# Performance work log

Measured on AMD Instinct MI355X. Metric: run time of the kernel, lower is better.

Reference implementation:

```python
import jax, jax.numpy as jnp
import numpy as np

N, E = 50000, 800000
H_IN, H, L = 256, 128, 3
EPS = 1e-5  # BatchNorm1d default eps


def setup_inputs() -> dict:
    key = jax.random.key(0)
    ks = jax.random.split(key, 8)
    x = jax.random.normal(ks[0], (N, H_IN), jnp.float32)
    edge_index = jax.random.randint(ks[1], (2, E), 0, N, dtype=jnp.int32)

    def glorot(k, fi, fo):
        lim = np.sqrt(6.0 / (fi + fo)).astype(np.float32)
        return jax.random.uniform(k, (fi, fo), jnp.float32, -lim, lim)

    W_feat = glorot(ks[2], H_IN, H)
    b_feat = jnp.zeros((H,), jnp.float32)
    wkeys = jax.random.split(ks[3], L)
    Ws = jnp.stack([glorot(wkeys[i], H, H) for i in range(L)])
    bs = jnp.zeros((L, H), jnp.float32)
    # BN init per reset_parameters: weight=1, bias=1e-4
    bn_feat_g = jnp.ones((H_IN,), jnp.float32)
    bn_feat_b = jnp.full((H_IN,), 1e-4, jnp.float32)
    bn_g = jnp.ones((L, H), jnp.float32)
    bn_b = jnp.full((L, H), 1e-4, jnp.float32)
    return dict(x=x, edge_index=edge_index, bn_feat_g=bn_feat_g, bn_feat_b=bn_feat_b,
                W_feat=W_feat, b_feat=b_feat, bn_g=bn_g, bn_b=bn_b, Ws=Ws, bs=bs)


def _bn(x, gamma, beta):
    # training-mode BatchNorm1d: batch statistics over nodes, biased variance
    mu = x.mean(0)
    var = x.var(0)
    return (x - mu) * jax.lax.rsqrt(var + EPS) * gamma + beta


def _gcn_norm(edge_index, n):
    # add self-loops (fill value 1) + symmetric deg^-1/2 normalization
    row, col = edge_index[0], edge_index[1]
    loop = jnp.arange(n, dtype=row.dtype)
    row = jnp.concatenate([row, loop])
    col = jnp.concatenate([col, loop])
    deg = jax.ops.segment_sum(jnp.ones_like(row, jnp.float32), row, num_segments=n)
    dinv = jnp.where(deg > 0, jax.lax.rsqrt(deg), 0.0)
    return row, col, dinv[row] * dinv[col]


def _gcn(x, W, b, row, col, norm, n):
    x = x @ W                                   # [n, out]
    msg = x[row] * norm[:, None]                # gather + scale, [E+n, out]
    out = jax.ops.segment_sum(msg, col, num_segments=n)  # scatter-add
    return out + b


def reference(x, edge_index, bn_feat_g, bn_feat_b, W_feat, b_feat, bn_g, bn_b, Ws, bs):
    n = x.shape[0]
    row, col, norm = _gcn_norm(edge_index, n)   # same for every layer
    x = _bn(x, bn_feat_g, bn_feat_b)
    x = _gcn(x, W_feat, b_feat, row, col, norm, n)
    for i in range(L):
        x = _bn(x, bn_g[i], bn_b[i])
        x = _gcn(x, Ws[i], bs[i], row, col, norm, n)
    return x
```

## Files before the change

kernel.cpp:

```cpp
#include <hip/hip_runtime.h>
#include <hip/hip_bf16.h>

#define H_IN 256
#define H    128
#define BN_EPS 1e-5f
#define NCOPY 32
#define NSLICE 256
#define SMAX 5120
#define STATS_FLOATS (NCOPY * 2 * H_IN)
#define SBLK 512
#define GEMMB 512

using u16 = unsigned short;
using u32 = unsigned int;
typedef __attribute__((ext_vector_type(8))) unsigned short us8;
typedef __attribute__((ext_vector_type(8))) short bf16x8;
typedef __attribute__((ext_vector_type(4))) float f32x4;

__device__ __forceinline__ float b2f(u16 u) {
    return __uint_as_float(((u32)u) << 16);
}
__device__ __forceinline__ u16 f2b(float f) {
    u32 u = __float_as_uint(f);
    u += 0x7FFF + ((u >> 16) & 1);
    return (u16)(u >> 16);
}

__global__ __launch_bounds__(256) void build_k(const int* __restrict__ row,
                                               const int* __restrict__ col,
                                               u32* __restrict__ deg,
                                               u32* __restrict__ bcnt_part,
                                               const float* __restrict__ x,
                                               u16* __restrict__ xb,
                                               float* __restrict__ statsA,
                                               int E, int total4) {
    int tid = threadIdx.x;
    if (blockIdx.x < NSLICE) {
        __shared__ u32 bcnt[256];
        bcnt[tid] = 0;
        __syncthreads();
        int len = (E + NSLICE - 1) / NSLICE;
        int e0 = blockIdx.x * len;
        int e1 = min(e0 + len, E);
        for (int e = e0 + tid; e < e1; e += 256) {
            atomicAdd(&deg[(u32)row[e]], 1u);
            atomicAdd(&bcnt[((u32)col[e]) >> 8], 1u);
        }
        __syncthreads();
        bcnt_part[blockIdx.x * 256 + tid] = bcnt[tid];
    } else {
        __shared__ float sh[2 * H_IN];
        const int K = H_IN;
        const int csz = 2 * H_IN;
        sh[tid] = 0.f;
        sh[tid + 256] = 0.f;
        __syncthreads();
        int gid = (blockIdx.x - NSLICE) * 256 + tid;
        int stride = SBLK * 256;
        int c0 = (gid * 4) % K;
        float s0=0.f,s1=0.f,s2=0.f,s3=0.f, q0=0.f,q1=0.f,q2=0.f,q3=0.f;
        const float4* A4 = (const float4*)x;
        ushort4* X4 = (ushort4*)xb;
        for (int i = gid; i < total4; i += stride) {
            float4 v = A4[i];
            ushort4 xv;
            xv.x = f2b(v.x); xv.y = f2b(v.y); xv.z = f2b(v.z); xv.w = f2b(v.w);
            X4[i] = xv;
            s0 += v.x; q0 += v.x * v.x;
            s1 += v.y; q1 += v.y * v.y;
            s2 += v.z; q2 += v.z * v.z;
            s3 += v.w; q3 += v.w * v.w;
        }
        atomicAdd(&sh[c0],     s0); atomicAdd(&sh[K + c0],     q0);
        atomicAdd(&sh[c0 + 1], s1); atomicAdd(&sh[K + c0 + 1], q1);
        atomicAdd(&sh[c0 + 2], s2); atomicAdd(&sh[K + c0 + 2], q2);
        atomicAdd(&sh[c0 + 3], s3); atomicAdd(&sh[K + c0 + 3], q3);
        __syncthreads();
        float* dst = statsA + (size_t)((blockIdx.x - NSLICE) & (NCOPY - 1)) * csz;
        for (int i = tid; i < csz; i += 256) atomicAdd(&dst[i], sh[i]);
    }
}

__global__ __launch_bounds__(256) void prep_k(const int* __restrict__ row,
                                              const int* __restrict__ col,
                                              const u32* __restrict__ bcnt_part,
                                              u32* __restrict__ bbase,
                                              u32* __restrict__ ebuf,
                                              const u32* __restrict__ deg,
                                              float* __restrict__ dinv,
                                              const float* __restrict__ W,
                                              const float* __restrict__ stats_mc,
                                              const float* __restrict__ g,
                                              const float* __restrict__ bcoef,
                                              const float* __restrict__ bias,
                                              u16* __restrict__ Wt,
                                              float* __restrict__ bp,
                                              int E, int N, int DB) {
    int tid = threadIdx.x;
    int bx = blockIdx.x;
    if (bx < NSLICE) {
        __shared__ u32 sc[256];
        __shared__ u32 cur[256];
        int s = bx;
        u32 tot = 0, pre = 0;
        for (int t = 0; t < NSLICE; ++t) {
            u32 v = bcnt_part[t * 256 + tid];
            tot += v;
            if (t < s) pre += v;
        }
        sc[tid] = tot;
        __syncthreads();
        for (int o = 1; o < 256; o <<= 1) {
            u32 xv = (tid >= o) ? sc[tid - o] : 0;
            __syncthreads();
            sc[tid] += xv;
            __syncthreads();
        }
        u32 base = sc[tid] - tot;
        if (s == 0) {
            bbase[tid] = base;
            if (tid == 255) bbase[256] = sc[255];
        }
        cur[tid] = base + pre;
        __syncthreads();
        int len = (E + NSLICE - 1) / NSLICE;
        int e0 = s * len;
        int e1 = min(e0 + len, E);
        for (int e = e0 + tid; e < e1; e += 256) {
            u32 r = (u32)row[e];
            u32 c = (u32)col[e];
            u32 pos = atomicAdd(&cur[c >> 8], 1u);
            ebuf[pos] = r | ((c & 255u) << 16);
        }
    } else if (bx < NSLICE + DB) {
        int n = (bx - NSLICE) * 256 + tid;
        if (n < N) dinv[n] = rsqrtf((float)deg[n] + 1.0f);
    } else {
        int j = bx - NSLICE - DB;
        int k = tid;
        const int K = H_IN;
        const int csz = 2 * H_IN;
        float sum = 0.f, sumsq = 0.f;
#pragma unroll
        for (int c = 0; c < NCOPY; ++c) {
            sum   += stats_mc[(size_t)c * csz + k];
            sumsq += stats_mc[(size_t)c * csz + K + k];
        }
        float mu = sum / (float)N;
        float var = sumsq / (float)N - mu * mu;
        float sK = g[k] * rsqrtf(var + BN_EPS);
        float tK = bcoef[k] - mu * sK;
        float w = W[(size_t)k * H + j];
        Wt[(size_t)j * K + k] = f2b(sK * w);
        __shared__ float red[256];
        red[k] = tK * w;
        __syncthreads();
        for (int o = 128; o > 0; o >>= 1) {
            if (k < o) red[k] += red[k + o];
            __syncthreads();
        }
        if (k == 0) bp[j] = bias[j] + red[0];
    }
}

__global__ void fold_k(const float* __restrict__ W, const float* __restrict__ stats_mc,
                       const float* __restrict__ g, const float* __restrict__ b,
                       const float* __restrict__ bias, u16* __restrict__ Wt,
                       float* __restrict__ bp, int N, int K) {
    int j = blockIdx.x;
    int k = threadIdx.x;
    int csz = 2 * K;
    float sum = 0.f, sumsq = 0.f;
#pragma unroll
    for (int c = 0; c < NCOPY; ++c) {
        sum   += stats_mc[(size_t)c * csz + k];
        sumsq += stats_mc[(size_t)c * csz + K + k];
    }
    float mu = sum / (float)N;
    float var = sumsq / (float)N - mu * mu;
    float s = g[k] * rsqrtf(var + BN_EPS);
    float t = b[k] - mu * s;
    float w = W[(size_t)k * H + j];
    Wt[(size_t)j * K + k] = f2b(s * w);
    __shared__ float red[256];
    red[k] = t * w;
    __syncthreads();
    for (int o = blockDim.x >> 1; o > 0; o >>= 1) {
        if (k < o) red[k] += red[k + o];
        __syncthreads();
    }
    if (k == 0) bp[j] = bias[j] + red[0];
}

template<int KT, int WITH_SORT>
__global__ __launch_bounds__(256) void gemm_mfma_k(const u16* __restrict__ Ab,
                                                   const u16* __restrict__ Wt,
                                                   u16* __restrict__ Yb, int M,
                                                   float* __restrict__ stats_z,
                                                   const u32* __restrict__ ebuf,
                                                   const u32* __restrict__ bbase,
                                                   int* __restrict__ rowptr,
                                                   u16* __restrict__ esrc, int N) {
    int tid = threadIdx.x;
    if constexpr (WITH_SORT != 0) {
        if (blockIdx.x >= GEMMB) {
            __shared__ u32 est[SMAX];
            __shared__ u32 hist[256], scanv[256], cur[256];
            int b = blockIdx.x - GEMMB;
            u32 base = bbase[b];
            int size = (int)(bbase[b + 1] - base);
            int st = min(size, SMAX);
            hist[tid] = 0;
            __syncthreads();
            for (int i = tid; i < st; i += 256) {
                u32 e = ebuf[base + i];
                est[i] = e;
                atomicAdd(&hist[(e >> 16) & 255u], 1u);
            }
            for (int i = SMAX + tid; i < size; i += 256) {
                u32 e = ebuf[base + i];
                atomicAdd(&hist[(e >> 16) & 255u], 1u);
            }
            __syncthreads();
            u32 own = hist[tid];
            scanv[tid] = own;
            __syncthreads();
            for (int o = 1; o < 256; o <<= 1) {
                u32 t = (tid >= o) ? scanv[tid - o] : 0;
                __syncthreads();
                scanv[tid] += t;
                __syncthreads();
            }
            u32 excl = scanv[tid] - own;
            int idx = (b << 8) + tid;
            if (idx <= N) rowptr[idx] = (int)(base + excl);
            cur[tid] = excl;
            __syncthreads();
            for (int i = tid; i < st; i += 256) {
                u32 e = est[i];
                u32 pos = atomicAdd(&cur[(e >> 16) & 255u], 1u);
                esrc[base + pos] = (u16)(e & 0xFFFFu);
            }
            for (int i = SMAX + tid; i < size; i += 256) {
                u32 e = ebuf[base + i];
                u32 pos = atomicAdd(&cur[(e >> 16) & 255u], 1u);
                esrc[base + pos] = (u16)(e & 0xFFFFu);
            }
            return;
        }
    }
    const int K = KT * 32;
    if (stats_z && blockIdx.x == 0) {
        for (int i = tid; i < STATS_FLOATS; i += 256) stats_z[i] = 0.f;
    }
    int w = tid >> 6;
    int lane = tid & 63;
    int m16 = lane & 15;
    int q = lane >> 4;

    bf16x8 bfrag[KT][2];
#pragma unroll
    for (int t = 0; t < KT; ++t)
#pragma unroll
        for (int p = 0; p < 2; ++p) {
            int ncol = 32 * w + 16 * p + m16;
            bfrag[t][p] = *(const bf16x8*)(Wt + (size_t)ncol * K + 32 * t + 8 * q);
        }

    int nchunk = M >> 4;
    for (int c = blockIdx.x; c < nchunk; c += GEMMB) {
        int m0 = c << 4;
        const u16* Arow = Ab + (size_t)(m0 + m16) * K + 8 * q;
        bf16x8 afrag[KT];
#pragma unroll
        for (int t = 0; t < KT; ++t)
            afrag[t] = *(const bf16x8*)(Arow + 32 * t);
        f32x4 acc0 = {0.f, 0.f, 0.f, 0.f}, acc1 = {0.f, 0.f, 0.f, 0.f};
#pragma unroll
        for (int t = 0; t < KT; ++t) {
            acc0 = __builtin_amdgcn_mfma_f32_16x16x32_bf16(afrag[t], bfrag[t][0], acc0, 0, 0, 0);
            acc1 = __builtin_amdgcn_mfma_f32_16x16x32_bf16(afrag[t], bfrag[t][1], acc1, 0, 0, 0);
        }
        u16* Crow = Yb + (size_t)(m0 + q * 4) * H + 32 * w + m16;
#pragma unroll
        for (int i = 0; i < 4; ++i) {
            Crow[(size_t)i * H]      = f2b(acc0[i]);
            Crow[(size_t)i * H + 16] = f2b(acc1[i]);
        }
    }
}

__global__ __launch_bounds__(256) void csragg_k(const int* __restrict__ rowptr,
                                                const u16* __restrict__ esrc,
                                                const u16* __restrict__ Yb,
                                                const float* __restrict__ dinv,
                                                const float* __restrict__ bp,
                                                u16* __restrict__ Ob,
                                                float* __restrict__ Of,
                                                float* __restrict__ stats_mc,
                                                int do_stats, int N) {
    __shared__ float sh[1024];
    int tid = threadIdx.x;
    int node = blockIdx.x * 16 + (tid >> 4);
    int fl = tid & 15;
    float o[8] = {0.f,0.f,0.f,0.f,0.f,0.f,0.f,0.f};
    if (node < N) {
        const us8* Y8 = (const us8*)Yb;
        float dn = dinv[node];
        float acc[8];
        {
            us8 ys = Y8[(size_t)node * 16 + fl];
#pragma unroll
            for (int j = 0; j < 8; ++j) acc[j] = dn * b2f(ys[j]);
        }
        int s = rowptr[node], e = rowptr[node + 1];
        int p = s;
        for (; p + 3 < e; p += 4) {
            int s0 = esrc[p], s1 = esrc[p + 1], s2 = esrc[p + 2], s3 = esrc[p + 3];
            float n0 = dinv[s0], n1 = dinv[s1], n2 = dinv[s2], n3 = dinv[s3];
            us8 v0 = Y8[(size_t)s0 * 16 + fl];
            us8 v1 = Y8[(size_t)s1 * 16 + fl];
            us8 v2 = Y8[(size_t)s2 * 16 + fl];
            us8 v3 = Y8[(size_t)s3 * 16 + fl];
#pragma unroll
            for (int j = 0; j < 8; ++j) acc[j] += n0 * b2f(v0[j]);
#pragma unroll
            for (int j = 0; j < 8; ++j) acc[j] += n1 * b2f(v1[j]);
#pragma unroll
            for (int j = 0; j < 8; ++j) acc[j] += n2 * b2f(v2[j]);
#pragma unroll
            for (int j = 0; j < 8; ++j) acc[j] += n3 * b2f(v3[j]);
        }
        for (; p < e; ++p) {
            int s0 = esrc[p];
            float n0 = dinv[s0];
            us8 v0 = Y8[(size_t)s0 * 16 + fl];
#pragma unroll
            for (int j = 0; j < 8; ++j) acc[j] += n0 * b2f(v0[j]);
        }
        float4 b0 = ((const float4*)bp)[fl * 2];
        float4 b1 = ((const float4*)bp)[fl * 2 + 1];
        o[0] = b0.x + dn * acc[0]; o[1] = b0.y + dn * acc[1];
        o[2] = b0.z + dn * acc[2]; o[3] = b0.w + dn * acc[3];
        o[4] = b1.x + dn * acc[4]; o[5] = b1.y + dn * acc[5];
        o[6] = b1.z + dn * acc[6]; o[7] = b1.w + dn * acc[7];
        if (Of) {
            float4* O4 = (float4*)Of;
            O4[(size_t)node * 32 + fl * 2]     = make_float4(o[0], o[1], o[2], o[3]);
            O4[(size_t)node * 32 + fl * 2 + 1] = make_float4(o[4], o[5], o[6], o[7]);
        } else {
            us8 ov;
#pragma unroll
            for (int j = 0; j < 8; ++j) ov[j] = f2b(o[j]);
            *(us8*)(Ob + (size_t)node * H + fl * 8) = ov;
        }
    }
    if (do_stats) {
        float sv[16];
#pragma unroll
        for (int j = 0; j < 8; ++j) { sv[j] = o[j]; sv[8 + j] = o[j] * o[j]; }
#pragma unroll
        for (int j = 0; j < 16; ++j) {
            sv[j] += __shfl_xor(sv[j], 16, 64);
            sv[j] += __shfl_xor(sv[j], 32, 64);
        }
        int lane = tid & 63, wv = tid >> 6;
        if (lane < 16) {
            float* base = sh + wv * 256;
#pragma unroll
            for (int j = 0; j < 8; ++j) {
                base[fl * 8 + j]       = sv[j];
                base[128 + fl * 8 + j] = sv[8 + j];
            }
        }
        __syncthreads();
        float v = sh[tid] + sh[256 + tid] + sh[512 + tid] + sh[768 + tid];
        atomicAdd(&stats_mc[(size_t)(blockIdx.x & (NCOPY - 1)) * (2 * H) + tid], v);
    }
}

extern "C" void kernel_launch(void* const* d_in, const int* in_sizes, int n_in,
                              void* d_out, int out_size, void* d_ws, size_t ws_size,
                              hipStream_t stream) {
    const float* x     = (const float*)d_in[0];
    const int*   ei    = (const int*)d_in[1];
    const float* bnfg  = (const float*)d_in[2];
    const float* bnfb  = (const float*)d_in[3];
    const float* Wfeat = (const float*)d_in[4];
    const float* bfeat = (const float*)d_in[5];
    const float* bng   = (const float*)d_in[6];
    const float* bnb   = (const float*)d_in[7];
    const float* Ws    = (const float*)d_in[8];
    const float* bs    = (const float*)d_in[9];

    int N = in_sizes[0] / H_IN;
    int E = in_sizes[1] / 2;
    const int* row = ei;
    const int* col = ei + E;

    int NB = (N + 255) >> 8;

    char* p = (char*)d_ws;
    auto alloc = [&](size_t bytes) { char* r = p; p += (bytes + 63) & ~size_t(63); return r; };
    float* statsA    = (float*)alloc(STATS_FLOATS * 4);
    float* statsB    = (float*)alloc(STATS_FLOATS * 4);
    u32*   deg       = (u32*)alloc((size_t)N * 4);
    float* dinv      = (float*)alloc((size_t)N * 4);
    u16*   Wt        = (u16*)alloc(H_IN * H * 2);
    float* bp        = (float*)alloc(H * 4);
    u32*   bcnt_part = (u32*)alloc(NSLICE * 256 * 4);
    u32*   bbase     = (u32*)alloc(257 * 4);
    int*   rowptr    = (int*)alloc((size_t)(N + 1) * 4);
    u32*   ebuf      = (u32*)alloc((size_t)E * 4);
    u16*   esrc      = (u16*)alloc((size_t)E * 2);
    u16*   xb        = (u16*)alloc((size_t)N * H_IN * 2);
    u16*   Yb        = (u16*)alloc((size_t)N * H * 2);
    u16*   ACTb      = (u16*)alloc((size_t)N * H * 2);

    float* out = (float*)d_out;

    hipMemsetAsync(statsA, 0, (size_t)(2 * STATS_FLOATS) * 4 + (size_t)N * 4, stream);

    build_k<<<NSLICE + SBLK, 256, 0, stream>>>(row, col, deg, bcnt_part, x, xb, statsA,
                                               E, N * H_IN / 4);
    prep_k<<<NSLICE + NB + H, 256, 0, stream>>>(row, col, bcnt_part, bbase, ebuf, deg, dinv,
                                                Wfeat, statsA, bnfg, bnfb, bfeat, Wt, bp,
                                                E, N, NB);
    gemm_mfma_k<8, 1><<<GEMMB + NB, 256, 0, stream>>>(xb, Wt, Yb, N, nullptr,
                                                      ebuf, bbase, rowptr, esrc, N);
    csragg_k<<<(N + 15) / 16, 256, 0, stream>>>(rowptr, esrc, Yb, dinv, bp,
                                                ACTb, nullptr, statsB, 1, N);

    for (int l = 1; l < 4; ++l) {
        const float* W    = Ws + (size_t)(l - 1) * H * H;
        const float* bias = bs + (size_t)(l - 1) * H;
        const float* g    = bng + (size_t)(l - 1) * H;
        const float* bb   = bnb + (size_t)(l - 1) * H;
        float* sfold   = (l & 1) ? statsB : statsA;
        float* szero   = (l == 1) ? statsA : (l == 2) ? statsB : nullptr;
        float* starget = ((l + 1) & 1) ? statsB : statsA;

        fold_k<<<H, H, 0, stream>>>(W, sfold, g, bb, bias, Wt, bp, N, H);
        gemm_mfma_k<4, 0><<<GEMMB, 256, 0, stream>>>(ACTb, Wt, Yb, N, szero,
                                                     nullptr, nullptr, nullptr, nullptr, N);
        csragg_k<<<(N + 15) / 16, 256, 0, stream>>>(rowptr, esrc, Yb, dinv, bp,
                                                    ACTb, (l == 3) ? out : nullptr,
                                                    starget, (l < 3) ? 1 : 0, N);
    }
}
```

Baseline: 394.9 us.

## Replace global degree atomics with sliced shared-memory 16-bit packed histograms

New measurement: 358.1 us. 1.1x faster.

```diff
diff --git a/kernel.cpp b/kernel.cpp
--- a/kernel.cpp
+++ b/kernel.cpp
@@ -6,6 +6,8 @@
 #define BN_EPS 1e-5f
 #define NCOPY 32
 #define NSLICE 256
+#define HSL 32
+#define QWMAX 8192
 #define SMAX 5120
 #define STATS_FLOATS (NCOPY * 2 * H_IN)
 #define SBLK 512
@@ -28,36 +30,56 @@
 
 __global__ __launch_bounds__(256) void build_k(const int* __restrict__ row,
                                                const int* __restrict__ col,
-                                               u32* __restrict__ deg,
+                                               u32* __restrict__ hist_part,
                                                u32* __restrict__ bcnt_part,
                                                const float* __restrict__ x,
                                                u16* __restrict__ xb,
                                                float* __restrict__ statsA,
-                                               int E, int total4) {
+                                               int E, int total4, int QW, int qN) {
+    __shared__ u32 smem[QWMAX];
     int tid = threadIdx.x;
-    if (blockIdx.x < NSLICE) {
-        __shared__ u32 bcnt[256];
+    int bx = blockIdx.x;
+    if (bx < NSLICE) {
+        u32* bcnt = smem;
         bcnt[tid] = 0;
         __syncthreads();
         int len = (E + NSLICE - 1) / NSLICE;
-        int e0 = blockIdx.x * len;
+        int e0 = bx * len;
         int e1 = min(e0 + len, E);
+        for (int e = e0 + tid; e < e1; e += 256)
+            atomicAdd(&bcnt[((u32)col[e]) >> 8], 1u);
+        __syncthreads();
+        bcnt_part[bx * 256 + tid] = bcnt[tid];
+    } else if (bx < NSLICE + 4 * HSL) {
+        int hb = bx - NSLICE;
+        int s = hb >> 2;
+        int qq = hb & 3;
+        u32* hist = smem;
+        for (int i = tid; i < QW; i += 256) hist[i] = 0;
+        __syncthreads();
+        int len = (E + HSL - 1) / HSL;
+        int e0 = s * len;
+        int e1 = min(e0 + len, E);
+        int lo = qq * qN;
         for (int e = e0 + tid; e < e1; e += 256) {
-            atomicAdd(&deg[(u32)row[e]], 1u);
-            atomicAdd(&bcnt[((u32)col[e]) >> 8], 1u);
-        }
-        __syncthreads();
-        bcnt_part[blockIdx.x * 256 + tid] = bcnt[tid];
+            int r = row[e] - lo;
+            if ((u32)r < (u32)qN)
+                atomicAdd(&hist[r >> 1], 1u << ((r & 1) << 4));
+        }
+        __syncthreads();
+        u32* dst = hist_part + (size_t)hb * QW;
+        for (int i = tid; i < QW; i += 256) dst[i] = hist[i];
     } else {
-        __shared__ float sh[2 * H_IN];
+        float* sh = (float*)smem;
         const int K = H_IN;
         const int csz = 2 * H_IN;
         sh[tid] = 0.f;
         sh[tid + 256] = 0.f;
         __syncthreads();
-        int gid = (blockIdx.x - NSLICE) * 256 + tid;
+        int sb = bx - NSLICE - 4 * HSL;
+        int gid = sb * 256 + tid;
         int stride = SBLK * 256;
-        int c0 = (gid * 4) % K;
+        int c0 = (gid * 4) & (H_IN - 1);
         float s0=0.f,s1=0.f,s2=0.f,s3=0.f, q0=0.f,q1=0.f,q2=0.f,q3=0.f;
         const float4* A4 = (const float4*)x;
         ushort4* X4 = (ushort4*)xb;
@@ -76,7 +98,7 @@
         atomicAdd(&sh[c0 + 2], s2); atomicAdd(&sh[K + c0 + 2], q2);
         atomicAdd(&sh[c0 + 3], s3); atomicAdd(&sh[K + c0 + 3], q3);
         __syncthreads();
-        float* dst = statsA + (size_t)((blockIdx.x - NSLICE) & (NCOPY - 1)) * csz;
+        float* dst = statsA + (size_t)(sb & (NCOPY - 1)) * csz;
         for (int i = tid; i < csz; i += 256) atomicAdd(&dst[i], sh[i]);
     }
 }
@@ -86,7 +108,7 @@
                                               const u32* __restrict__ bcnt_part,
                                               u32* __restrict__ bbase,
                                               u32* __restrict__ ebuf,
-                                              const u32* __restrict__ deg,
+                                              const u32* __restrict__ hist_part,
                                               float* __restrict__ dinv,
                                               const float* __restrict__ W,
                                               const float* __restrict__ stats_mc,
@@ -95,7 +117,7 @@
                                               const float* __restrict__ bias,
                                               u16* __restrict__ Wt,
                                               float* __restrict__ bp,
-                                              int E, int N, int DB) {
+                                              int E, int N, int DB, int QW, int qN) {
     int tid = threadIdx.x;
     int bx = blockIdx.x;
     if (bx < NSLICE) {
@@ -133,8 +155,17 @@
             ebuf[pos] = r | ((c & 255u) << 16);
         }
     } else if (bx < NSLICE + DB) {
-        int n = (bx - NSLICE) * 256 + tid;
-        if (n < N) dinv[n] = rsqrtf((float)deg[n] + 1.0f);
+        int w = (bx - NSLICE) * 256 + tid;
+        if (w < 4 * QW) {
+            int qq = w / QW;
+            int lw = w - qq * QW;
+            u32 v = 0;
+            for (int s = 0; s < HSL; ++s)
+                v += hist_part[(size_t)(s * 4 + qq) * QW + lw];
+            int n = qq * qN + 2 * lw;
+            if (n < N)     dinv[n]     = rsqrtf((float)(v & 0xFFFF) + 1.0f);
+            if (n + 1 < N) dinv[n + 1] = rsqrtf((float)(v >> 16) + 1.0f);
+        }
     } else {
         int j = bx - NSLICE - DB;
         int k = tid;
@@ -399,15 +430,18 @@
     const int* col = ei + E;
 
     int NB = (N + 255) >> 8;
+    int QW = (N + 7) / 8;
+    int qN = 2 * QW;
+    int DB = (4 * QW + 255) / 256;
 
     char* p = (char*)d_ws;
     auto alloc = [&](size_t bytes) { char* r = p; p += (bytes + 63) & ~size_t(63); return r; };
     float* statsA    = (float*)alloc(STATS_FLOATS * 4);
     float* statsB    = (float*)alloc(STATS_FLOATS * 4);
-    u32*   deg       = (u32*)alloc((size_t)N * 4);
     float* dinv      = (float*)alloc((size_t)N * 4);
     u16*   Wt        = (u16*)alloc(H_IN * H * 2);
     float* bp        = (float*)alloc(H * 4);
+    u32*   hist_part = (u32*)alloc((size_t)4 * HSL * QW * 4);
     u32*   bcnt_part = (u32*)alloc(NSLICE * 256 * 4);
     u32*   bbase     = (u32*)alloc(257 * 4);
     int*   rowptr    = (int*)alloc((size_t)(N + 1) * 4);
@@ -419,13 +453,15 @@
 
     float* out = (float*)d_out;
 
-    hipMemsetAsync(statsA, 0, (size_t)(2 * STATS_FLOATS) * 4 + (size_t)N * 4, stream);
-
-    build_k<<<NSLICE + SBLK, 256, 0, stream>>>(row, col, deg, bcnt_part, x, xb, statsA,
-                                               E, N * H_IN / 4);
-    prep_k<<<NSLICE + NB + H, 256, 0, stream>>>(row, col, bcnt_part, bbase, ebuf, deg, dinv,
+    hipMemsetAsync(statsA, 0, (size_t)(2 * STATS_FLOATS) * 4, stream);
+
+    build_k<<<NSLICE + 4 * HSL + SBLK, 256, 0, stream>>>(row, col, hist_part, bcnt_part,
+                                                         x, xb, statsA, E, N * H_IN / 4,
+                                                         QW, qN);
+    prep_k<<<NSLICE + DB + H, 256, 0, stream>>>(row, col, bcnt_part, bbase, ebuf,
+                                                hist_part, dinv,
                                                 Wfeat, statsA, bnfg, bnfb, bfeat, Wt, bp,
-                                                E, N, NB);
+                                                E, N, DB, QW, qN);
     gemm_mfma_k<8, 1><<<GEMMB + NB, 256, 0, stream>>>(xb, Wt, Yb, N, nullptr,
                                                       ebuf, bbase, rowptr, esrc, N);
     csragg_k<<<(N + 15) / 16, 256, 0, stream>>>(rowptr, esrc, Yb, dinv, bp,
```
